# Kernel optimization log

Measured on AMD Instinct MI355X. Metric: run time of the kernel, lower is better.

The kernel has to match this reference:

```python
import jax, jax.numpy as jnp
import numpy as np

HC = 64                 # half_context
PAD = HC + 3            # padding_idx row of positional table
NEG = 1.0e12            # additive mask constant from the torch code


def setup_inputs() -> dict:
    key = jax.random.key(0)
    ks = jax.random.split(key, 7)
    B, S, D, C = 32, 2048, 1024, 256
    embeds = jax.random.normal(ks[0], (B, S, D), dtype=jnp.float32)
    embeds_mask = jnp.ones((B, S), dtype=jnp.float32)
    latent = jax.random.normal(ks[1], (C, D), dtype=jnp.float32)
    att_diag = jax.random.normal(ks[2], (D,), dtype=jnp.float32)
    tok_diag = jax.random.normal(ks[3], (D,), dtype=jnp.float32)
    pos_table = jax.random.normal(ks[4], (2 * HC + 4, D), dtype=jnp.float32)
    pos_table = pos_table.at[PAD].set(0.0)  # padding_idx row is zeros
    tok_mult = jnp.ones((1,), dtype=jnp.float32)
    rel_pos_ids = jax.random.randint(ks[5], (B, S), 0, HC + 4, dtype=jnp.int32)
    return {
        "embeds": embeds,
        "embeds_mask": embeds_mask,
        "latent": latent,
        "att_diag": att_diag,
        "tok_diag": tok_diag,
        "pos_table": pos_table,
        "tok_mult": tok_mult,
        "rel_pos_ids": rel_pos_ids,
    }


def reference(embeds, embeds_mask, latent, att_diag, tok_diag, pos_table, tok_mult, rel_pos_ids):
    # positional-embedding gather and merge (dropouts are identity in eval)
    absolute_pos = rel_pos_ids + HC                       # [B,S]
    pos_embeds = pos_table[absolute_pos]                  # [B,S,D]
    merged = tok_mult[0] * embeds + pos_embeds            # [B,S,D]
    # entity-token attention scores: (latent * diag) @ merged^T
    scores = jnp.einsum('cd,bsd->bcs', latent * att_diag, merged)  # [B,C,S]
    m = embeds_mask[:, None, :]                           # [B,1,S]
    scores = scores * m + (m - 1.0) * NEG                 # mask-add
    top = jnp.max(scores, axis=1)                         # max over classes -> [B,S]
    att_probs = jax.nn.softmax(top, axis=1)               # softmax over tokens
    # weighted sum of (embeds * tok_diag) by attention probs -> [B,D]
    ctx_vecs = jnp.einsum('bsd,d,bs->bd', embeds, tok_diag, att_probs)
    return ctx_vecs
```

## Files before the change

### kernel.cpp

```cpp
#include <hip/hip_runtime.h>
#include <hip/hip_bf16.h>


#define HC 64
#define NEGV 1000000000000.0f

constexpr int Bb = 32, Ss = 2048, Dd = 1024, Cc = 256;
constexpr int NKC = 32;
constexpr int CT = Cc / 16;
constexpr int NBLK = 16;

typedef _Float16 f16x8 __attribute__((ext_vector_type(8)));
typedef float    f32x4 __attribute__((ext_vector_type(4)));

__global__ __launch_bounds__(256) void k_prep_w(
    const float* __restrict__ latent, const float* __restrict__ att_diag,
    _Float16* __restrict__ whi)
{
    const int idx = blockIdx.x * 256 + threadIdx.x;
    const int c = idx >> 10, k = idx & 1023;
    const float wv = latent[idx] * att_diag[k];
    const int kc = k >> 5, g = (k >> 3) & 3, i = k & 7;
    const int lane = (c & 15) + 16 * g, ct = c >> 4;
    whi[(size_t)kc * 8192 + (size_t)ct * 512 + lane * 8 + i] = (_Float16)wv;
}

__global__ __launch_bounds__(256, 2) void k_scores_mfma(
    const float* __restrict__ embeds,
    const float* __restrict__ mask,
    const float* __restrict__ pos_table,
    const float* __restrict__ tok_mult,
    const int*   __restrict__ rel_ids,
    const _Float16* __restrict__ whi,
    float* __restrict__ partial,
    float* __restrict__ mblk,
    float* __restrict__ zblk)
{
    __shared__ _Float16 sbuf[2][8192];
    __shared__ float l_sh[128];
    __shared__ float w_sh[128];
    __shared__ float red2[2];
    __shared__ float zred[2];

    const int t  = threadIdx.x;
    const int wv = t >> 6;
    const int l  = t & 63;
    const int lr = l & 15;
    const int lg = l >> 4;

    const int b   = blockIdx.x >> 4;
    const int blk = blockIdx.x & 15;
    const int s0  = blk * 128;

    const float tm = tok_mult[0];

    const float* erow[2];
    const float* prow[2];
    #pragma unroll
    for (int st = 0; st < 2; st++) {
        const int tok = s0 + wv * 32 + st * 16 + lr;
        erow[st] = embeds + ((size_t)b * Ss + tok) * Dd;
        prow[st] = pos_table + (size_t)(rel_ids[b * Ss + tok] + HC) * Dd;
    }

    f32x4 acc[CT][2];
    #pragma unroll
    for (int ct = 0; ct < CT; ct++)
        #pragma unroll
        for (int st = 0; st < 2; st++) acc[ct][st] = (f32x4){0.f, 0.f, 0.f, 0.f};

    f32x4 e0[2], e1[2], p0[2], p1[2];
    auto loadEP = [&](int kc) {
        const int k0 = kc * 32 + lg * 8;
        #pragma unroll
        for (int st = 0; st < 2; st++) {
            e0[st] = *(const f32x4*)(erow[st] + k0);
            e1[st] = *(const f32x4*)(erow[st] + k0 + 4);
            p0[st] = *(const f32x4*)(prow[st] + k0);
            p1[st] = *(const f32x4*)(prow[st] + k0 + 4);
        }
    };

    auto stage = [&](int kc, _Float16* dst) {
        const _Float16* src = whi + (size_t)kc * 8192;
        #pragma unroll
        for (int i = 0; i < 4; i++) {
            const int off = (i * 4 + wv) << 9;
            __builtin_amdgcn_global_load_lds(
                (const __attribute__((address_space(1))) void*)(src + off + l * 8),
                (__attribute__((address_space(3))) void*)(dst + off),
                16, 0, 0);
        }
    };

    stage(0, sbuf[0]);
    loadEP(0);
    asm volatile("s_waitcnt vmcnt(8)" ::: "memory");
    __builtin_amdgcn_s_barrier();

    int cur = 0;
    for (int kc = 0; kc < NKC; kc++) {
        if (kc + 1 < NKC) stage(kc + 1, sbuf[cur ^ 1]);

        f16x8 bh[2], bl[2];
        #pragma unroll
        for (int st = 0; st < 2; st++) {
            float e[8], p[8];
            *(f32x4*)&e[0] = e0[st]; *(f32x4*)&e[4] = e1[st];
            *(f32x4*)&p[0] = p0[st]; *(f32x4*)&p[4] = p1[st];
            #pragma unroll
            for (int i = 0; i < 8; i++) {
                const float x = fmaf(tm, e[i], p[i]);
                const _Float16 h = (_Float16)x;
                bh[st][i] = h;
                bl[st][i] = (_Float16)(x - (float)h);
            }
        }
        if (kc + 1 < NKC) loadEP(kc + 1);

        const _Float16* base = sbuf[cur];
        #pragma unroll
        for (int ct = 0; ct < CT; ct++) {
            const f16x8 ah = *(const f16x8*)(base + ct * 512 + l * 8);
            #pragma unroll
            for (int st = 0; st < 2; st++) {
                acc[ct][st] = __builtin_amdgcn_mfma_f32_16x16x32_f16(ah, bh[st], acc[ct][st], 0, 0, 0);
                acc[ct][st] = __builtin_amdgcn_mfma_f32_16x16x32_f16(ah, bl[st], acc[ct][st], 0, 0, 0);
            }
        }
        asm volatile("s_waitcnt vmcnt(8)" ::: "memory");
        __builtin_amdgcn_s_barrier();
        cur ^= 1;
    }

    #pragma unroll
    for (int st = 0; st < 2; st++) {
        float mx = acc[0][st][0];
        #pragma unroll
        for (int ct = 0; ct < CT; ct++)
            #pragma unroll
            for (int r = 0; r < 4; r++) mx = fmaxf(mx, acc[ct][st][r]);
        mx = fmaxf(mx, __shfl_xor(mx, 16));
        mx = fmaxf(mx, __shfl_xor(mx, 32));
        if (lg == 0) {
            const int si = wv * 32 + st * 16 + lr;
            const int s  = s0 + si;
            const float mk = mask[b * Ss + s];
            l_sh[si] = mx * mk + (mk - 1.0f) * NEGV;
        }
    }
    __syncthreads();

    if (t < 128) {
        float v = l_sh[t];
        #pragma unroll
        for (int o = 32; o >= 1; o >>= 1) v = fmaxf(v, __shfl_xor(v, o));
        if ((t & 63) == 0) red2[t >> 6] = v;
    }
    __syncthreads();
    const float Mb = fmaxf(red2[0], red2[1]);
    if (t < 128) w_sh[t] = expf(l_sh[t] - Mb);
    __syncthreads();
    if (t < 128) {
        float z = w_sh[t];
        #pragma unroll
        for (int o = 32; o >= 1; o >>= 1) z += __shfl_xor(z, o);
        if ((t & 63) == 0) zred[t >> 6] = z;
    }
    __syncthreads();

    {
        const float* eb = embeds + ((size_t)b * Ss + s0) * Dd + t * 4;
        f32x4 ca = (f32x4){0.f, 0.f, 0.f, 0.f};
        #pragma unroll 8
        for (int s = 0; s < 128; s++) {
            const float wgt = w_sh[s];
            const f32x4 ev = *(const f32x4*)(eb + (size_t)s * Dd);
            ca[0] = fmaf(wgt, ev[0], ca[0]);
            ca[1] = fmaf(wgt, ev[1], ca[1]);
            ca[2] = fmaf(wgt, ev[2], ca[2]);
            ca[3] = fmaf(wgt, ev[3], ca[3]);
        }
        *(f32x4*)(partial + ((size_t)(b * NBLK + blk)) * Dd + t * 4) = ca;
        if (t == 0) {
            mblk[b * NBLK + blk] = Mb;
            zblk[b * NBLK + blk] = zred[0] + zred[1];
        }
    }
}

__global__ __launch_bounds__(256) void k_finish(
    const float* __restrict__ mblk, const float* __restrict__ zblk,
    const float* __restrict__ partial, const float* __restrict__ tok_diag,
    float* __restrict__ out)
{
    __shared__ float cf[NBLK];
    const int b = blockIdx.x, t = threadIdx.x;

    if (t < 64) {
        const float mv = (t < NBLK) ? mblk[b * NBLK + t] : -3.4e38f;
        float M = mv;
        #pragma unroll
        for (int o = 32; o >= 1; o >>= 1) M = fmaxf(M, __shfl_xor(M, o));
        const float zv = (t < NBLK) ? zblk[b * NBLK + t] * expf(mv - M) : 0.f;
        float Z = zv;
        #pragma unroll
        for (int o = 32; o >= 1; o >>= 1) Z += __shfl_xor(Z, o);
        if (t < NBLK) cf[t] = expf(mv - M) / Z;
    }
    __syncthreads();

    const int d = t * 4;
    f32x4 a = (f32x4){0.f, 0.f, 0.f, 0.f};
    #pragma unroll
    for (int j = 0; j < NBLK; j++) {
        const float c = cf[j];
        const f32x4 p = *(const f32x4*)(partial + ((size_t)(b * NBLK + j)) * Dd + d);
        a[0] = fmaf(c, p[0], a[0]);
        a[1] = fmaf(c, p[1], a[1]);
        a[2] = fmaf(c, p[2], a[2]);
        a[3] = fmaf(c, p[3], a[3]);
    }
    const f32x4 td = *(const f32x4*)(tok_diag + d);
    f32x4 o = a * td;
    *(f32x4*)(out + (size_t)b * Dd + d) = o;
}

extern "C" void kernel_launch(void* const* d_in, const int* in_sizes, int n_in,
                              void* d_out, int out_size, void* d_ws, size_t ws_size,
                              hipStream_t stream) {
    const float* embeds    = (const float*)d_in[0];
    const float* mask      = (const float*)d_in[1];
    const float* latent    = (const float*)d_in[2];
    const float* att_diag  = (const float*)d_in[3];
    const float* tok_diag  = (const float*)d_in[4];
    const float* pos_table = (const float*)d_in[5];
    const float* tok_mult  = (const float*)d_in[6];
    const int*   rel_ids   = (const int*)d_in[7];
    float* out = (float*)d_out;

    char* ws = (char*)d_ws;
    _Float16* whi    = (_Float16*)(ws);
    float*    partial= (float*)(ws + 524288);
    float*    mblk   = (float*)(ws + 2621440);
    float*    zblk   = (float*)(ws + 2623488);

    k_prep_w<<<(Cc * Dd) / 256, 256, 0, stream>>>(latent, att_diag, whi);
    k_scores_mfma<<<Bb * NBLK, 256, 0, stream>>>(
        embeds, mask, pos_table, tok_mult, rel_ids, whi, partial, mblk, zblk);
    k_finish<<<Bb, 256, 0, stream>>>(mblk, zblk, partial, tok_diag, out);
}
```

Baseline: 121.9 us.

## Load weight fragments directly from global memory and drop LDS double buffering

The async global-to-LDS staging of the fp16 weight matrix and the per-iteration barrier are removed. Each wave now reads its weight fragments straight from global memory, relying on L2/L1 caching since every block re-reads the same 512KB. The embed/pos loads get explicit two-deep register ping-pong buffering in an unrolled-by-two loop. This removes LDS traffic and block-wide sync, but adds global load latency on the MFMA path and raises register pressure.

```diff
diff --git a/kernel.cpp b/kernel.cpp
--- a/kernel.cpp
+++ b/kernel.cpp
@@ -22,7 +22,7 @@
     const float wv = latent[idx] * att_diag[k];
     const int kc = k >> 5, g = (k >> 3) & 3, i = k & 7;
     const int lane = (c & 15) + 16 * g, ct = c >> 4;
-    whi[(size_t)kc * 8192 + (size_t)ct * 512 + lane * 8 + i] = (_Float16)wv;
+    whi[(size_t)(kc * CT + ct) * 512 + lane * 8 + i] = (_Float16)wv;
 }
 
 __global__ __launch_bounds__(256, 2) void k_scores_mfma(
@@ -36,11 +36,9 @@
     float* __restrict__ mblk,
     float* __restrict__ zblk)
 {
-    __shared__ _Float16 sbuf[2][8192];
     __shared__ float l_sh[128];
     __shared__ float w_sh[128];
-    __shared__ float red2[2];
-    __shared__ float zred[2];
+    __shared__ float red2[2], zred[2];
 
     const int t  = threadIdx.x;
     const int wv = t >> 6;
@@ -69,45 +67,39 @@
         #pragma unroll
         for (int st = 0; st < 2; st++) acc[ct][st] = (f32x4){0.f, 0.f, 0.f, 0.f};
 
-    f32x4 e0[2], e1[2], p0[2], p1[2];
-    auto loadEP = [&](int kc) {
+    f32x4 eA0[2], eA1[2], pA0[2], pA1[2];
+    f32x4 eB0[2], eB1[2], pB0[2], pB1[2];
+    auto loadA = [&](int kc) {
         const int k0 = kc * 32 + lg * 8;
         #pragma unroll
         for (int st = 0; st < 2; st++) {
-            e0[st] = *(const f32x4*)(erow[st] + k0);
-            e1[st] = *(const f32x4*)(erow[st] + k0 + 4);
-            p0[st] = *(const f32x4*)(prow[st] + k0);
-            p1[st] = *(const f32x4*)(prow[st] + k0 + 4);
+            eA0[st] = *(const f32x4*)(erow[st] + k0);
+            eA1[st] = *(const f32x4*)(erow[st] + k0 + 4);
+            pA0[st] = *(const f32x4*)(prow[st] + k0);
+            pA1[st] = *(const f32x4*)(prow[st] + k0 + 4);
         }
     };
-
-    auto stage = [&](int kc, _Float16* dst) {
-        const _Float16* src = whi + (size_t)kc * 8192;
-        #pragma unroll
-        for (int i = 0; i < 4; i++) {
-            const int off = (i * 4 + wv) << 9;
-            __builtin_amdgcn_global_load_lds(
-                (const __attribute__((address_space(1))) void*)(src + off + l * 8),
-                (__attribute__((address_space(3))) void*)(dst + off),
-                16, 0, 0);
+    auto loadB = [&](int kc) {
+        const int k0 = kc * 32 + lg * 8;
+        #pragma unroll
+        for (int st = 0; st < 2; st++) {
+            eB0[st] = *(const f32x4*)(erow[st] + k0);
+            eB1[st] = *(const f32x4*)(erow[st] + k0 + 4);
+            pB0[st] = *(const f32x4*)(prow[st] + k0);
+            pB1[st] = *(const f32x4*)(prow[st] + k0 + 4);
         }
     };
 
-    stage(0, sbuf[0]);
-    loadEP(0);
-    asm volatile("s_waitcnt vmcnt(8)" ::: "memory");
-    __builtin_amdgcn_s_barrier();
-
-    int cur = 0;
-    for (int kc = 0; kc < NKC; kc++) {
-        if (kc + 1 < NKC) stage(kc + 1, sbuf[cur ^ 1]);
-
+    const f16x8* whi8 = (const f16x8*)whi;
+
+    auto body = [&](int kc, const f32x4* E0, const f32x4* E1,
+                    const f32x4* P0, const f32x4* P1) {
         f16x8 bh[2], bl[2];
         #pragma unroll
         for (int st = 0; st < 2; st++) {
             float e[8], p[8];
-            *(f32x4*)&e[0] = e0[st]; *(f32x4*)&e[4] = e1[st];
-            *(f32x4*)&p[0] = p0[st]; *(f32x4*)&p[4] = p1[st];
+            *(f32x4*)&e[0] = E0[st]; *(f32x4*)&e[4] = E1[st];
+            *(f32x4*)&p[0] = P0[st]; *(f32x4*)&p[4] = P1[st];
             #pragma unroll
             for (int i = 0; i < 8; i++) {
                 const float x = fmaf(tm, e[i], p[i]);
@@ -116,21 +108,24 @@
                 bl[st][i] = (_Float16)(x - (float)h);
             }
         }
-        if (kc + 1 < NKC) loadEP(kc + 1);
-
-        const _Float16* base = sbuf[cur];
+        const int fbase = kc * (CT * 64) + l;
         #pragma unroll
         for (int ct = 0; ct < CT; ct++) {
-            const f16x8 ah = *(const f16x8*)(base + ct * 512 + l * 8);
+            const f16x8 ah = whi8[fbase + ct * 64];
             #pragma unroll
             for (int st = 0; st < 2; st++) {
                 acc[ct][st] = __builtin_amdgcn_mfma_f32_16x16x32_f16(ah, bh[st], acc[ct][st], 0, 0, 0);
                 acc[ct][st] = __builtin_amdgcn_mfma_f32_16x16x32_f16(ah, bl[st], acc[ct][st], 0, 0, 0);
             }
         }
-        asm volatile("s_waitcnt vmcnt(8)" ::: "memory");
-        __builtin_amdgcn_s_barrier();
-        cur ^= 1;
+    };
+
+    loadA(0);
+    for (int kc = 0; kc < NKC; kc += 2) {
+        if (kc + 1 < NKC) loadB(kc + 1);
+        body(kc, eA0, eA1, pA0, pA1);
+        if (kc + 2 < NKC) loadA(kc + 2);
+        body(kc + 1, eB0, eB1, pB0, pB1);
     }
 
     #pragma unroll
```

Result: slower. 149.4 us (+22.5%).
